# Kernel tuning notes

Measured on AMD Instinct MI355X. Metric: run time of the kernel, lower is better.

Reference implementation:

```python
import jax, jax.numpy as jnp
import numpy as np

H = 32  # hidden size fixed by the module


def setup_inputs() -> dict:
    key = jax.random.key(0)
    ks = jax.random.split(key, 7)
    B, T, D = 1024, 512, 64
    s_ih = 1.0 / np.sqrt(H)
    return {
        "x": jax.random.normal(ks[0], (B, T, D), dtype=jnp.float32),
        "W_ih": jax.random.normal(ks[1], (3 * H, D), dtype=jnp.float32) * s_ih,
        "W_hh": jax.random.normal(ks[2], (3 * H, H), dtype=jnp.float32) * s_ih,
        "b_ih": jax.random.normal(ks[3], (3 * H,), dtype=jnp.float32) * s_ih,
        "b_hh": jax.random.normal(ks[4], (3 * H,), dtype=jnp.float32) * s_ih,
        "W_fc": jax.random.normal(ks[5], (1, H), dtype=jnp.float32) * s_ih,
        "b_fc": jax.random.normal(ks[6], (1,), dtype=jnp.float32) * s_ih,
    }


def _gru_last_hidden(x, W_ih, W_hh, b_ih, b_hh):
    # Precompute input-side gates for all timesteps in one big GEMM: [B,T,3H]
    xg = jnp.einsum("btd,gd->btg", x, W_ih) + b_ih
    xg = jnp.swapaxes(xg, 0, 1)  # [T,B,3H] for scan
    B = x.shape[0]
    h0 = jnp.zeros((B, H), dtype=x.dtype)

    def step(h, xg_t):
        gh = h @ W_hh.T + b_hh  # [B,3H]
        xr, xz, xn = xg_t[:, :H], xg_t[:, H:2 * H], xg_t[:, 2 * H:]
        hr, hz, hn = gh[:, :H], gh[:, H:2 * H], gh[:, 2 * H:]
        r = jax.nn.sigmoid(xr + hr)
        z = jax.nn.sigmoid(xz + hz)
        n = jnp.tanh(xn + r * hn)
        h_new = (1.0 - z) * n + z * h
        return h_new, None

    h_last, _ = jax.lax.scan(step, h0, xg)
    return h_last  # [B,H]


def reference(x, W_ih, W_hh, b_ih, b_hh, W_fc, b_fc):
    # GRU -> dropout (eval mode: identity) -> Linear on last timestep
    h_last = _gru_last_hidden(x, W_ih, W_hh, b_ih, b_hh)
    return h_last @ W_fc.T + b_fc  # [B,1]
```

## Files before the change

### kernel.cpp

```cpp
#include <hip/hip_runtime.h>

#define TS 512
#define DD 64
#define HH 32

typedef _Float16 half2v __attribute__((ext_vector_type(2)));

__device__ __forceinline__ float fdot2(half2v a, half2v b, float c) {
#if __has_builtin(__builtin_amdgcn_fdot2)
    return __builtin_amdgcn_fdot2(a, b, c, false);
#else
    return fmaf((float)a[0], (float)b[0], fmaf((float)a[1], (float)b[1], c));
#endif
}

__device__ __forceinline__ float fast_sigmoid(float a) {
    return __builtin_amdgcn_rcpf(1.0f + __expf(-a));
}

__device__ __forceinline__ half2v h2(unsigned int u) {
    return __builtin_bit_cast(half2v, u);
}

__global__ __launch_bounds__(64)
__attribute__((amdgpu_waves_per_eu(1, 1)))
void gru_fused(
    const float* __restrict__ x,
    const float* __restrict__ Wih,
    const float* __restrict__ Whh,
    const float* __restrict__ bih,
    const float* __restrict__ bhh,
    const float* __restrict__ Wfc,
    const float* __restrict__ bfc,
    float* __restrict__ out)
{
    __shared__ __align__(16) _Float16 xs16[4][DD];
    __shared__ __align__(16) _Float16 hs16[HH];

    const int b    = blockIdx.x;
    const int lane = threadIdx.x;
    const int s    = lane >> 5;
    const int h    = lane & 31;

    half2v wr2[16], wz2[16], wn2[16];
    {
        const float4* pr = reinterpret_cast<const float4*>(Wih + (0 * HH + h) * DD + s * 32);
        const float4* pz = reinterpret_cast<const float4*>(Wih + (1 * HH + h) * DD + s * 32);
        const float4* pn = reinterpret_cast<const float4*>(Wih + (2 * HH + h) * DD + s * 32);
#pragma unroll
        for (int k = 0; k < 8; ++k) {
            float4 a = pr[k];
            wr2[2*k]   = half2v{(_Float16)a.x, (_Float16)a.y};
            wr2[2*k+1] = half2v{(_Float16)a.z, (_Float16)a.w};
            float4 c = pz[k];
            wz2[2*k]   = half2v{(_Float16)c.x, (_Float16)c.y};
            wz2[2*k+1] = half2v{(_Float16)c.z, (_Float16)c.w};
            float4 e = pn[k];
            wn2[2*k]   = half2v{(_Float16)e.x, (_Float16)e.y};
            wn2[2*k+1] = half2v{(_Float16)e.z, (_Float16)e.w};
        }
    }
    half2v ur2[8], uz2[8], un2[8];
    {
        const float4* pr = reinterpret_cast<const float4*>(Whh + (0 * HH + h) * HH + s * 16);
        const float4* pz = reinterpret_cast<const float4*>(Whh + (1 * HH + h) * HH + s * 16);
        const float4* pn = reinterpret_cast<const float4*>(Whh + (2 * HH + h) * HH + s * 16);
#pragma unroll
        for (int k = 0; k < 4; ++k) {
            float4 a = pr[k];
            ur2[2*k]   = half2v{(_Float16)a.x, (_Float16)a.y};
            ur2[2*k+1] = half2v{(_Float16)a.z, (_Float16)a.w};
            float4 c = pz[k];
            uz2[2*k]   = half2v{(_Float16)c.x, (_Float16)c.y};
            uz2[2*k+1] = half2v{(_Float16)c.z, (_Float16)c.w};
            float4 e = pn[k];
            un2[2*k]   = half2v{(_Float16)e.x, (_Float16)e.y};
            un2[2*k+1] = half2v{(_Float16)e.z, (_Float16)e.w};
        }
    }

    const float br  = bih[h]          + bhh[h];
    const float bz  = bih[HH + h]     + bhh[HH + h];
    const float bxn = bih[2 * HH + h];
    const float bhn = bhh[2 * HH + h];
    const float wfc = Wfc[h];
    const float bf0 = bfc[0];

    const float* xrow = x + (size_t)b * TS * DD;

    float p0 = xrow[0 * DD + lane];
    float p1 = xrow[1 * DD + lane];
    float p2 = xrow[2 * DD + lane];
    float ra = xrow[3 * DD + lane];
    float rb = xrow[4 * DD + lane];
    float rc = xrow[5 * DD + lane];
    xs16[0][lane] = (_Float16)p0;
    xs16[1][lane] = (_Float16)p1;
    xs16[2][lane] = (_Float16)p2;
    __builtin_amdgcn_wave_barrier();

    float h_own = 0.0f;
    half2v hv2[8];
#pragma unroll
    for (int k = 0; k < 8; ++k) hv2[k] = half2v{(_Float16)0.0f, (_Float16)0.0f};

    float ar, az, an;
    {
        const uint4* xp = reinterpret_cast<const uint4*>(&xs16[0][s * 32]);
        ar = 0.f; az = 0.f; an = 0.f;
#pragma unroll
        for (int k = 0; k < 4; ++k) {
            uint4 q = xp[k];
            half2v v0 = h2(q.x), v1 = h2(q.y), v2 = h2(q.z), v3 = h2(q.w);
            ar = fdot2(wr2[4*k  ], v0, ar);
            az = fdot2(wz2[4*k  ], v0, az);
            an = fdot2(wn2[4*k  ], v0, an);
            ar = fdot2(wr2[4*k+1], v1, ar);
            az = fdot2(wz2[4*k+1], v1, az);
            an = fdot2(wn2[4*k+1], v1, an);
            ar = fdot2(wr2[4*k+2], v2, ar);
            az = fdot2(wz2[4*k+2], v2, az);
            an = fdot2(wn2[4*k+2], v2, an);
            ar = fdot2(wr2[4*k+3], v3, ar);
            az = fdot2(wz2[4*k+3], v3, az);
            an = fdot2(wn2[4*k+3], v3, an);
        }
    }

    for (int t = 0; t < TS; ++t) {
        xs16[(t + 3) & 3][lane] = (_Float16)ra;
        ra = rb; rb = rc;
        int tf = t + 6; if (tf > TS - 1) tf = TS - 1;
        rc = xrow[tf * DD + lane];

        float gr = 0.f, gz = 0.f, gn = 0.f;
#pragma unroll
        for (int k = 0; k < 8; ++k) {
            gr = fdot2(ur2[k], hv2[k], gr);
            gz = fdot2(uz2[k], hv2[k], gz);
            gn = fdot2(un2[k], hv2[k], gn);
        }

        float tr = ar + gr;  tr += __shfl_xor(tr, 32);
        float tz = az + gz;  tz += __shfl_xor(tz, 32);
        float txn = an + __shfl_xor(an, 32);
        float tgn = gn + __shfl_xor(gn, 32);

        float r = fast_sigmoid(tr + br);
        float z = fast_sigmoid(tz + bz);
        float npre = txn + bxn + r * (tgn + bhn);
        npre = fminf(fmaxf(npre, -30.f), 30.f);
        float e2 = __expf(-2.f * npre);
        float n = (1.f - e2) * __builtin_amdgcn_rcpf(1.f + e2);
        h_own = n + z * (h_own - n);

        hs16[h] = (_Float16)h_own;
        __builtin_amdgcn_wave_barrier();
        {
            const uint4* hp = reinterpret_cast<const uint4*>(&hs16[s * 16]);
            uint4 q0 = hp[0];
            uint4 q1 = hp[1];
            hv2[0] = h2(q0.x);
            hv2[1] = h2(q0.y);
            hv2[2] = h2(q0.z);
            hv2[3] = h2(q0.w);
            hv2[4] = h2(q1.x);
            hv2[5] = h2(q1.y);
            hv2[6] = h2(q1.z);
            hv2[7] = h2(q1.w);
        }

        if (t + 1 < TS) {
            const uint4* xp = reinterpret_cast<const uint4*>(&xs16[(t + 1) & 3][s * 32]);
            ar = 0.f; az = 0.f; an = 0.f;
#pragma unroll
            for (int k = 0; k < 4; ++k) {
                uint4 q = xp[k];
                half2v v0 = h2(q.x), v1 = h2(q.y), v2 = h2(q.z), v3 = h2(q.w);
                ar = fdot2(wr2[4*k  ], v0, ar);
                az = fdot2(wz2[4*k  ], v0, az);
                an = fdot2(wn2[4*k  ], v0, an);
                ar = fdot2(wr2[4*k+1], v1, ar);
                az = fdot2(wz2[4*k+1], v1, az);
                an = fdot2(wn2[4*k+1], v1, an);
                ar = fdot2(wr2[4*k+2], v2, ar);
                az = fdot2(wz2[4*k+2], v2, az);
                an = fdot2(wn2[4*k+2], v2, an);
                ar = fdot2(wr2[4*k+3], v3, ar);
                az = fdot2(wz2[4*k+3], v3, az);
                an = fdot2(wn2[4*k+3], v3, an);
            }
        }
    }

    float v = h_own * wfc;
#pragma unroll
    for (int off = 32; off >= 1; off >>= 1) v += __shfl_xor(v, off);
    if (lane == 0) out[b] = 0.5f * v + bf0;
}

extern "C" void kernel_launch(void* const* d_in, const int* in_sizes, int n_in,
                              void* d_out, int out_size, void* d_ws, size_t ws_size,
                              hipStream_t stream) {
    const float* x    = (const float*)d_in[0];
    const float* Wih  = (const float*)d_in[1];
    const float* Whh  = (const float*)d_in[2];
    const float* bih  = (const float*)d_in[3];
    const float* bhh  = (const float*)d_in[4];
    const float* Wfc  = (const float*)d_in[5];
    const float* bfc  = (const float*)d_in[6];
    float* out = (float*)d_out;

    const int B = in_sizes[0] / (TS * DD);
    gru_fused<<<dim3(B), dim3(64), 0, stream>>>(x, Wih, Whh, bih, bhh, Wfc, bfc, out);
}
```

Before: 185.3 us.

## Map one sequence per half-wave, removing cross-half reductions

```diff
diff --git a/kernel.cpp b/kernel.cpp
--- a/kernel.cpp
+++ b/kernel.cpp
@@ -24,7 +24,7 @@
 
 __global__ __launch_bounds__(64)
 __attribute__((amdgpu_waves_per_eu(1, 1)))
-void gru_fused(
+void gru_fused2(
     const float* __restrict__ x,
     const float* __restrict__ Wih,
     const float* __restrict__ Whh,
@@ -34,21 +34,21 @@
     const float* __restrict__ bfc,
     float* __restrict__ out)
 {
-    __shared__ __align__(16) _Float16 xs16[4][DD];
-    __shared__ __align__(16) _Float16 hs16[HH];
-
-    const int b    = blockIdx.x;
+    __shared__ __align__(16) _Float16 xs16[2][4][DD];
+    __shared__ __align__(16) _Float16 hs16[2][HH];
+
     const int lane = threadIdx.x;
-    const int s    = lane >> 5;
+    const int p    = lane >> 5;
     const int h    = lane & 31;
-
-    half2v wr2[16], wz2[16], wn2[16];
+    const int b    = blockIdx.x * 2 + p;
+
+    half2v wr2[32], wz2[32], wn2[32];
     {
-        const float4* pr = reinterpret_cast<const float4*>(Wih + (0 * HH + h) * DD + s * 32);
-        const float4* pz = reinterpret_cast<const float4*>(Wih + (1 * HH + h) * DD + s * 32);
-        const float4* pn = reinterpret_cast<const float4*>(Wih + (2 * HH + h) * DD + s * 32);
-#pragma unroll
-        for (int k = 0; k < 8; ++k) {
+        const float4* pr = reinterpret_cast<const float4*>(Wih + (0 * HH + h) * DD);
+        const float4* pz = reinterpret_cast<const float4*>(Wih + (1 * HH + h) * DD);
+        const float4* pn = reinterpret_cast<const float4*>(Wih + (2 * HH + h) * DD);
+#pragma unroll
+        for (int k = 0; k < 16; ++k) {
             float4 a = pr[k];
             wr2[2*k]   = half2v{(_Float16)a.x, (_Float16)a.y};
             wr2[2*k+1] = half2v{(_Float16)a.z, (_Float16)a.w};
@@ -60,13 +60,13 @@
             wn2[2*k+1] = half2v{(_Float16)e.z, (_Float16)e.w};
         }
     }
-    half2v ur2[8], uz2[8], un2[8];
+    half2v ur2[16], uz2[16], un2[16];
     {
-        const float4* pr = reinterpret_cast<const float4*>(Whh + (0 * HH + h) * HH + s * 16);
-        const float4* pz = reinterpret_cast<const float4*>(Whh + (1 * HH + h) * HH + s * 16);
-        const float4* pn = reinterpret_cast<const float4*>(Whh + (2 * HH + h) * HH + s * 16);
-#pragma unroll
-        for (int k = 0; k < 4; ++k) {
+        const float4* pr = reinterpret_cast<const float4*>(Whh + (0 * HH + h) * HH);
+        const float4* pz = reinterpret_cast<const float4*>(Whh + (1 * HH + h) * HH);
+        const float4* pn = reinterpret_cast<const float4*>(Whh + (2 * HH + h) * HH);
+#pragma unroll
+        for (int k = 0; k < 8; ++k) {
             float4 a = pr[k];
             ur2[2*k]   = half2v{(_Float16)a.x, (_Float16)a.y};
             ur2[2*k+1] = half2v{(_Float16)a.z, (_Float16)a.w};
@@ -86,117 +86,104 @@
     const float wfc = Wfc[h];
     const float bf0 = bfc[0];
 
-    const float* xrow = x + (size_t)b * TS * DD;
-
-    float p0 = xrow[0 * DD + lane];
-    float p1 = xrow[1 * DD + lane];
-    float p2 = xrow[2 * DD + lane];
-    float ra = xrow[3 * DD + lane];
-    float rb = xrow[4 * DD + lane];
-    float rc = xrow[5 * DD + lane];
-    xs16[0][lane] = (_Float16)p0;
-    xs16[1][lane] = (_Float16)p1;
-    xs16[2][lane] = (_Float16)p2;
+    const float2* xr2 = reinterpret_cast<const float2*>(x + (size_t)b * TS * DD);
+
+    float2 q0 = xr2[0 * 32 + h];
+    float2 q1 = xr2[1 * 32 + h];
+    float2 q2 = xr2[2 * 32 + h];
+    float2 ra = xr2[3 * 32 + h];
+    float2 rb = xr2[4 * 32 + h];
+    float2 rc = xr2[5 * 32 + h];
+    *reinterpret_cast<half2v*>(&xs16[p][0][2 * h]) = half2v{(_Float16)q0.x, (_Float16)q0.y};
+    *reinterpret_cast<half2v*>(&xs16[p][1][2 * h]) = half2v{(_Float16)q1.x, (_Float16)q1.y};
+    *reinterpret_cast<half2v*>(&xs16[p][2][2 * h]) = half2v{(_Float16)q2.x, (_Float16)q2.y};
     __builtin_amdgcn_wave_barrier();
 
     float h_own = 0.0f;
-    half2v hv2[8];
-#pragma unroll
-    for (int k = 0; k < 8; ++k) hv2[k] = half2v{(_Float16)0.0f, (_Float16)0.0f};
+    half2v hv2[16];
+#pragma unroll
+    for (int k = 0; k < 16; ++k) hv2[k] = half2v{(_Float16)0.0f, (_Float16)0.0f};
 
     float ar, az, an;
     {
-        const uint4* xp = reinterpret_cast<const uint4*>(&xs16[0][s * 32]);
-        ar = 0.f; az = 0.f; an = 0.f;
-#pragma unroll
-        for (int k = 0; k < 4; ++k) {
+        const uint4* xp = reinterpret_cast<const uint4*>(&xs16[p][0][0]);
+        float a0 = 0.f, a1 = 0.f, c0 = 0.f, c1 = 0.f, e0 = 0.f, e1 = 0.f;
+#pragma unroll
+        for (int k = 0; k < 8; ++k) {
             uint4 q = xp[k];
             half2v v0 = h2(q.x), v1 = h2(q.y), v2 = h2(q.z), v3 = h2(q.w);
-            ar = fdot2(wr2[4*k  ], v0, ar);
-            az = fdot2(wz2[4*k  ], v0, az);
-            an = fdot2(wn2[4*k  ], v0, an);
-            ar = fdot2(wr2[4*k+1], v1, ar);
-            az = fdot2(wz2[4*k+1], v1, az);
-            an = fdot2(wn2[4*k+1], v1, an);
-            ar = fdot2(wr2[4*k+2], v2, ar);
-            az = fdot2(wz2[4*k+2], v2, az);
-            an = fdot2(wn2[4*k+2], v2, an);
-            ar = fdot2(wr2[4*k+3], v3, ar);
-            az = fdot2(wz2[4*k+3], v3, az);
-            an = fdot2(wn2[4*k+3], v3, an);
-        }
+            a0 = fdot2(wr2[4*k  ], v0, a0);  a1 = fdot2(wr2[4*k+1], v1, a1);
+            c0 = fdot2(wz2[4*k  ], v0, c0);  c1 = fdot2(wz2[4*k+1], v1, c1);
+            e0 = fdot2(wn2[4*k  ], v0, e0);  e1 = fdot2(wn2[4*k+1], v1, e1);
+            a0 = fdot2(wr2[4*k+2], v2, a0);  a1 = fdot2(wr2[4*k+3], v3, a1);
+            c0 = fdot2(wz2[4*k+2], v2, c0);  c1 = fdot2(wz2[4*k+3], v3, c1);
+            e0 = fdot2(wn2[4*k+2], v2, e0);  e1 = fdot2(wn2[4*k+3], v3, e1);
+        }
+        ar = a0 + a1; az = c0 + c1; an = e0 + e1;
     }
 
     for (int t = 0; t < TS; ++t) {
-        xs16[(t + 3) & 3][lane] = (_Float16)ra;
+        *reinterpret_cast<half2v*>(&xs16[p][(t + 3) & 3][2 * h]) =
+            half2v{(_Float16)ra.x, (_Float16)ra.y};
         ra = rb; rb = rc;
         int tf = t + 6; if (tf > TS - 1) tf = TS - 1;
-        rc = xrow[tf * DD + lane];
-
-        float gr = 0.f, gz = 0.f, gn = 0.f;
+        rc = xr2[tf * 32 + h];
+
+        float gr0 = 0.f, gr1 = 0.f, gz0 = 0.f, gz1 = 0.f, gn0 = 0.f, gn1 = 0.f;
 #pragma unroll
         for (int k = 0; k < 8; ++k) {
-            gr = fdot2(ur2[k], hv2[k], gr);
-            gz = fdot2(uz2[k], hv2[k], gz);
-            gn = fdot2(un2[k], hv2[k], gn);
-        }
-
-        float tr = ar + gr;  tr += __shfl_xor(tr, 32);
-        float tz = az + gz;  tz += __shfl_xor(tz, 32);
-        float txn = an + __shfl_xor(an, 32);
-        float tgn = gn + __shfl_xor(gn, 32);
-
-        float r = fast_sigmoid(tr + br);
-        float z = fast_sigmoid(tz + bz);
-        float npre = txn + bxn + r * (tgn + bhn);
+            gr0 = fdot2(ur2[2*k  ], hv2[2*k  ], gr0);
+            gr1 = fdot2(ur2[2*k+1], hv2[2*k+1], gr1);
+            gz0 = fdot2(uz2[2*k  ], hv2[2*k  ], gz0);
+            gz1 = fdot2(uz2[2*k+1], hv2[2*k+1], gz1);
+            gn0 = fdot2(un2[2*k  ], hv2[2*k  ], gn0);
+            gn1 = fdot2(un2[2*k+1], hv2[2*k+1], gn1);
+        }
+
+        float r = fast_sigmoid(ar + gr0 + gr1 + br);
+        float z = fast_sigmoid(az + gz0 + gz1 + bz);
+        float npre = an + bxn + r * (gn0 + gn1 + bhn);
         npre = fminf(fmaxf(npre, -30.f), 30.f);
         float e2 = __expf(-2.f * npre);
         float n = (1.f - e2) * __builtin_amdgcn_rcpf(1.f + e2);
         h_own = n + z * (h_own - n);
 
-        hs16[h] = (_Float16)h_own;
+        hs16[p][h] = (_Float16)h_own;
         __builtin_amdgcn_wave_barrier();
         {
-            const uint4* hp = reinterpret_cast<const uint4*>(&hs16[s * 16]);
-            uint4 q0 = hp[0];
-            uint4 q1 = hp[1];
-            hv2[0] = h2(q0.x);
-            hv2[1] = h2(q0.y);
-            hv2[2] = h2(q0.z);
-            hv2[3] = h2(q0.w);
-            hv2[4] = h2(q1.x);
-            hv2[5] = h2(q1.y);
-            hv2[6] = h2(q1.z);
-            hv2[7] = h2(q1.w);
+            const uint4* hp = reinterpret_cast<const uint4*>(&hs16[p][0]);
+            uint4 h0 = hp[0];
+            uint4 h1 = hp[1];
+            uint4 h2q = hp[2];
+            uint4 h3 = hp[3];
+            hv2[ 0] = h2(h0.x);  hv2[ 1] = h2(h0.y);  hv2[ 2] = h2(h0.z);  hv2[ 3] = h2(h0.w);
+            hv2[ 4] = h2(h1.x);  hv2[ 5] = h2(h1.y);  hv2[ 6] = h2(h1.z);  hv2[ 7] = h2(h1.w);
+            hv2[ 8] = h2(h2q.x); hv2[ 9] = h2(h2q.y); hv2[10] = h2(h2q.z); hv2[11] = h2(h2q.w);
+            hv2[12] = h2(h3.x);  hv2[13] = h2(h3.y);  hv2[14] = h2(h3.z);  hv2[15] = h2(h3.w);
         }
 
         if (t + 1 < TS) {
-            const uint4* xp = reinterpret_cast<const uint4*>(&xs16[(t + 1) & 3][s * 32]);
-            ar = 0.f; az = 0.f; an = 0.f;
-#pragma unroll
-            for (int k = 0; k < 4; ++k) {
+            const uint4* xp = reinterpret_cast<const uint4*>(&xs16[p][(t + 1) & 3][0]);
+            float a0 = 0.f, a1 = 0.f, c0 = 0.f, c1 = 0.f, e0 = 0.f, e1 = 0.f;
+#pragma unroll
+            for (int k = 0; k < 8; ++k) {
                 uint4 q = xp[k];
                 half2v v0 = h2(q.x), v1 = h2(q.y), v2 = h2(q.z), v3 = h2(q.w);
-                ar = fdot2(wr2[4*k  ], v0, ar);
-                az = fdot2(wz2[4*k  ], v0, az);
-                an = fdot2(wn2[4*k  ], v0, an);
-                ar = fdot2(wr2[4*k+1], v1, ar);
-                az = fdot2(wz2[4*k+1], v1, az);
-                an = fdot2(wn2[4*k+1], v1, an);
-                ar = fdot2(wr2[4*k+2], v2, ar);
-                az = fdot2(wz2[4*k+2], v2, az);
-                an = fdot2(wn2[4*k+2], v2, an);
-                ar = fdot2(wr2[4*k+3], v3, ar);
-                az = fdot2(wz2[4*k+3], v3, az);
-                an = fdot2(wn2[4*k+3], v3, an);
+                a0 = fdot2(wr2[4*k  ], v0, a0);  a1 = fdot2(wr2[4*k+1], v1, a1);
+                c0 = fdot2(wz2[4*k  ], v0, c0);  c1 = fdot2(wz2[4*k+1], v1, c1);
+                e0 = fdot2(wn2[4*k  ], v0, e0);  e1 = fdot2(wn2[4*k+1], v1, e1);
+                a0 = fdot2(wr2[4*k+2], v2, a0);  a1 = fdot2(wr2[4*k+3], v3, a1);
+                c0 = fdot2(wz2[4*k+2], v2, c0);  c1 = fdot2(wz2[4*k+3], v3, c1);
+                e0 = fdot2(wn2[4*k+2], v2, e0);  e1 = fdot2(wn2[4*k+3], v3, e1);
             }
+            ar = a0 + a1; az = c0 + c1; an = e0 + e1;
         }
     }
 
     float v = h_own * wfc;
 #pragma unroll
-    for (int off = 32; off >= 1; off >>= 1) v += __shfl_xor(v, off);
-    if (lane == 0) out[b] = 0.5f * v + bf0;
+    for (int off = 16; off >= 1; off >>= 1) v += __shfl_xor(v, off);
+    if (h == 0) out[b] = v + bf0;
 }
 
 extern "C" void kernel_launch(void* const* d_in, const int* in_sizes, int n_in,
@@ -212,5 +199,5 @@
     float* out = (float*)d_out;
 
     const int B = in_sizes[0] / (TS * DD);
-    gru_fused<<<dim3(B), dim3(64), 0, stream>>>(x, Wih, Whh, bih, bhh, Wfc, bfc, out);
-}
+    gru_fused2<<<dim3(B / 2), dim3(64), 0, stream>>>(x, Wih, Whh, bih, bhh, Wfc, bfc, out);
+}
```

Result: slower. 239.7 us (+29.4%).
